# Kernel optimization log

Measured on AMD Instinct MI355X. Metric: run time of the kernel, lower is better.

Reference implementation:

```python
import jax, jax.numpy as jnp
import numpy as np

B, C, H, W = 4, 512, 64, 64
MID = C // 8  # 64


def setup_inputs() -> dict:
    key = jax.random.key(0)
    ks = jax.random.split(key, 8)
    s = 0.02
    return {
        "x": jax.random.normal(ks[0], (B, C, H, W), dtype=jnp.float32),
        "Wq": jax.random.normal(ks[1], (MID, C), dtype=jnp.float32) * s,
        "bq": jax.random.normal(ks[2], (MID,), dtype=jnp.float32) * s,
        "Wk": jax.random.normal(ks[3], (MID, C), dtype=jnp.float32) * s,
        "bk": jax.random.normal(ks[4], (MID,), dtype=jnp.float32) * s,
        "Wv": jax.random.normal(ks[5], (C, C), dtype=jnp.float32) * s,
        "bv": jax.random.normal(ks[6], (C,), dtype=jnp.float32) * s,
        "gamma": jax.random.uniform(ks[7], (1,), dtype=jnp.float32),
    }


def reference(x, Wq, bq, Wk, bk, Wv, bv, gamma):
    b, c, h, w = x.shape
    n = h * w
    xf = x.reshape(b, c, n)  # [B, C, N]
    # 1x1 convs are per-position linear maps
    q = jnp.einsum('mc,bcn->bnm', Wq, xf) + bq            # [B, N, mid]
    k = jnp.einsum('mc,bcn->bmn', Wk, xf) + bk[:, None]   # [B, mid, N]
    sim = jax.nn.softmax(jnp.einsum('bnm,bmj->bnj', q, k), axis=-1)  # [B, N, N]
    v = jnp.einsum('dc,bcn->bdn', Wv, xf) + bv[:, None]   # [B, C, N]
    # feat[:, d, i] = sum_j v[:, d, j] * sim[:, i, j]
    feat = jnp.einsum('bdj,bij->bdi', v, sim)             # [B, C, N]
    out = gamma[0] * feat + xf
    return out.reshape(b, c, h, w)
```

## Files before the change

### kernel.cpp

```cpp
#include <hip/hip_runtime.h>

#define BATCH 4
#define CCH   512
#define NN    4096
#define MIDD  64

typedef unsigned short u16;
typedef unsigned int   u32;
typedef short s8v  __attribute__((ext_vector_type(8)));
typedef float f16v __attribute__((ext_vector_type(16)));

__device__ __forceinline__ u16 f2bf(float f) {
  u32 u = __float_as_uint(f);
  u += 0x7fffu + ((u >> 16) & 1u);
  return (u16)(u >> 16);
}

__device__ __forceinline__ void g2lds16(const u16* g, u16* l) {
  __builtin_amdgcn_global_load_lds(
      (const __attribute__((address_space(1))) u32*)(const void*)g,
      (__attribute__((address_space(3))) u32*)(void*)l, 16, 0, 0);
}

#define S_WAITCNT(vm, lgkm) \
  __builtin_amdgcn_s_waitcnt(((vm) & 15) | (((vm) >> 4) << 14) | (0x7 << 4) | ((lgkm) << 8))

__global__ __launch_bounds__(256) void prep_w(
    const float* __restrict__ Wq, const float* __restrict__ Wk,
    const float* __restrict__ Wv, u16* __restrict__ Wb)
{
  int e = (blockIdx.x * 256 + threadIdx.x) * 8;
  const float* src;
  if (e < 64 * 512)       src = Wq + e;
  else if (e < 128 * 512) src = Wk + (e - 64 * 512);
  else                    src = Wv + (e - 128 * 512);
  float4 v0 = *(const float4*)src;
  float4 v1 = *(const float4*)(src + 4);
  uint4 p;
  p.x = (u32)f2bf(v0.x) | ((u32)f2bf(v0.y) << 16);
  p.y = (u32)f2bf(v0.z) | ((u32)f2bf(v0.w) << 16);
  p.z = (u32)f2bf(v1.x) | ((u32)f2bf(v1.y) << 16);
  p.w = (u32)f2bf(v1.z) | ((u32)f2bf(v1.w) << 16);
  *(uint4*)(Wb + e) = p;
}

__global__ __launch_bounds__(256) void transpose_cast(
    const float* __restrict__ x, u16* __restrict__ xbT)
{
  const int b  = blockIdx.z;
  const int c0 = blockIdx.y * 64;
  const int n0 = blockIdx.x * 64;
  const int t  = threadIdx.x;
  __shared__ float ts[64 * 65];

  #pragma unroll
  for (int k = 0; k < 4; k++) {
    int idx = t + 256 * k;
    int cc = idx >> 4, n4 = idx & 15;
    float4 v = *(const float4*)&x[((size_t)(b * CCH + c0 + cc)) * NN + n0 + n4 * 4];
    float* p = &ts[cc * 65 + n4 * 4];
    p[0] = v.x; p[1] = v.y; p[2] = v.z; p[3] = v.w;
  }
  __syncthreads();

  const int n = t >> 2, cb = (t & 3) * 16;
  u16 tmp[16];
  #pragma unroll
  for (int j = 0; j < 16; j++) tmp[j] = f2bf(ts[(cb + j) * 65 + n]);
  u16* dst = &xbT[((size_t)b * NN + n0 + n) * CCH + c0 + cb];
  *(uint4*)&dst[0] = *(uint4*)&tmp[0];
  *(uint4*)&dst[8] = *(uint4*)&tmp[8];
}

__global__ __launch_bounds__(256, 2) void proj_gemm(
    const u16* __restrict__ xbT, const u16* __restrict__ Wb,
    const float* __restrict__ bq, const float* __restrict__ bk,
    const float* __restrict__ bv,
    u16* __restrict__ qT, u16* __restrict__ kT, u16* __restrict__ vF)
{
  const int b  = blockIdx.z;
  const int mt = blockIdx.y;
  const int n0 = blockIdx.x * 256;
  const int t  = threadIdx.x;
  const int ln = t & 31, hi = (t & 63) >> 5, w = t >> 6;
  const int l  = t & 63;
  const int l2 = l & 3, lr = l >> 2;
  const int swc = (l2 ^ (lr & 3)) * 8;

  const int mrow0 = (mt < 8) ? (128 + mt * 64) : ((mt == 8) ? 0 : 64);
  const float* bias = (mt < 8) ? (bv + mt * 64) : ((mt == 8) ? bq : bk);

  __shared__ u16 ws[2][64 * 32];
  __shared__ u16 xs[2][256 * 32];

  const u16* xsrc = xbT + ((size_t)b * NN + n0 + w * 64 + lr) * CCH + swc;
  const u16* wsrc = Wb + (size_t)(mrow0 + w * 16 + lr) * 512 + swc;

  f16v acc[4];
  #pragma unroll
  for (int i = 0; i < 4; i++)
    #pragma unroll
    for (int r = 0; r < 16; r++) acc[i][r] = 0.f;

  #pragma unroll
  for (int i = 0; i < 4; i++)
    g2lds16(xsrc + (size_t)(16 * i) * CCH, &xs[0][(w * 64 + i * 16) * 32]);
  g2lds16(wsrc, &ws[0][w * 16 * 32]);

  for (int it = 0; it < 16; it++) {
    const int cur = it & 1, nxt = cur ^ 1;
    __builtin_amdgcn_s_barrier();
    const int c1 = ((it + 1) & 15) * 32;
    #pragma unroll
    for (int i = 0; i < 4; i++)
      g2lds16(xsrc + (size_t)(16 * i) * CCH + c1, &xs[nxt][(w * 64 + i * 16) * 32]);
    g2lds16(wsrc + c1, &ws[nxt][w * 16 * 32]);

    S_WAITCNT(5, 15);
    __builtin_amdgcn_s_barrier();

    #pragma unroll
    for (int ks = 0; ks < 2; ks++) {
      const int cb = ((2 * ks + hi) ^ (ln & 3)) << 3;
      s8v a0 = *(const s8v*)&ws[cur][(ln)           * 32 + cb];
      s8v a1 = *(const s8v*)&ws[cur][(32 + ln)      * 32 + cb];
      s8v b0 = *(const s8v*)&xs[cur][(w * 64 + ln)      * 32 + cb];
      s8v b1 = *(const s8v*)&xs[cur][(w * 64 + 32 + ln) * 32 + cb];
      acc[0] = __builtin_amdgcn_mfma_f32_32x32x16_bf16(a0, b0, acc[0], 0, 0, 0);
      acc[1] = __builtin_amdgcn_mfma_f32_32x32x16_bf16(a0, b1, acc[1], 0, 0, 0);
      acc[2] = __builtin_amdgcn_mfma_f32_32x32x16_bf16(a1, b0, acc[2], 0, 0, 0);
      acc[3] = __builtin_amdgcn_mfma_f32_32x32x16_bf16(a1, b1, acc[3], 0, 0, 0);
    }
  }

  S_WAITCNT(0, 0);
  __builtin_amdgcn_s_barrier();

  if (mt < 8) {
    u16* xt = &xs[0][0];
    #pragma unroll
    for (int mi = 0; mi < 2; mi++)
      #pragma unroll
      for (int ni = 0; ni < 2; ni++) {
        f16v& a = acc[mi * 2 + ni];
        #pragma unroll
        for (int r = 0; r < 16; r++) {
          int row = (r & 3) + 8 * (r >> 2) + 4 * hi;
          int m   = mi * 32 + row;
          int nr  = w * 64 + ni * 32 + ln;
          int c8  = nr >> 3;
          xt[m * 256 + ((c8 ^ (m & 31)) << 3) + (nr & 7)] = f2bf(a[r] + bias[m]);
        }
      }
    __syncthreads();
    const int jt0 = n0 >> 6;
    const size_t dgb = ((size_t)b * 64 + jt0 + w) * 16 + mt * 2;
    #pragma unroll
    for (int mh = 0; mh < 2; mh++)
      #pragma unroll
      for (int ks = 0; ks < 4; ks++) {
        int c8 = w * 8 + ks * 2 + hi;
        int m  = mh * 32 + ln;
        s8v vv = *(const s8v*)&xt[m * 256 + ((c8 ^ ln) << 3)];
        *(s8v*)&vF[(((dgb + mh) * 4 + ks) * 64 + l) * 8] = vv;
      }
  } else {
    u16* dst = (mt == 8) ? qT : kT;
    u16* xt  = &xs[0][0];
    #pragma unroll
    for (int mi = 0; mi < 2; mi++)
      #pragma unroll
      for (int ni = 0; ni < 2; ni++) {
        f16v& a = acc[mi * 2 + ni];
        #pragma unroll
        for (int r = 0; r < 16; r++) {
          int row = (r & 3) + 8 * (r >> 2) + 4 * hi;
          int m   = mi * 32 + row;
          int nr  = w * 64 + ni * 32 + ln;
          xt[(nr << 6) + (((m >> 3) ^ (ln & 7)) << 3) + (m & 7)] = f2bf(a[r] + bias[m]);
        }
      }
    __syncthreads();
    const int r7 = t & 7;
    u16* drow = &dst[((size_t)b * NN + n0 + t) * 64];
    #pragma unroll
    for (int k = 0; k < 8; k++)
      *(uint4*)&drow[k * 8] = *(uint4*)&xt[(t << 6) + ((k ^ r7) << 3)];
  }
}

__global__ __launch_bounds__(256, 2) void attn_kernel(
    const u16* __restrict__ qT,
    const u16* __restrict__ kT,
    const u16* __restrict__ vF,
    const float* __restrict__ x,
    const float* __restrict__ gamma,
    float* __restrict__ out)
{
  __shared__ u16 ksm[2][64 * 64];
  __shared__ u16 plm[2][64 * 64];

  const int bx    = blockIdx.x;
  const int slot  = bx & 7;
  const int b     = slot >> 1;
  const int dbase = (slot & 1) * 256;
  const int i0    = (bx >> 3) * 64;
  const int t     = threadIdx.x;
  const int l     = t & 63, ln = l & 31, hi = l >> 5;
  const int w     = t >> 6;
  const int qh    = w >> 1;
  const int jh    = w & 1;
  const int l3    = l & 7, lh3 = l >> 3;
  const int sw8   = (l3 ^ lh3) * 8;

  s8v qfrag[4];
  {
    const u16* qp = qT + ((size_t)b * NN + i0 + qh * 32 + ln) * 64 + hi * 8;
    #pragma unroll
    for (int k = 0; k < 4; k++) qfrag[k] = *(const s8v*)(qp + 16 * k);
  }

  const u16* kbase = kT + (size_t)b * NN * 64;
  const u16* ksrc  = kbase + (size_t)(16 * w + lh3) * 64 + sw8;
  const u16* vfb = vF + (size_t)b * (64 * 16 * 4 * 64 * 8);
  const int dg0  = (slot & 1) * 8 + w;

  f16v oacc[4];
  #pragma unroll
  for (int i = 0; i < 4; i++)
    #pragma unroll
    for (int r = 0; r < 16; r++) oacc[i][r] = 0.f;
  float lpart[16];
  #pragma unroll
  for (int r = 0; r < 16; r++) lpart[r] = 0.f;

  #pragma unroll
  for (int i = 0; i < 2; i++)
    g2lds16(ksrc + (size_t)(8 * i) * 64, &ksm[0][(w * 2 + i) * 512]);

  for (int it = 0; it < 64; it++) {
    const int cur = it & 1, nxt = cur ^ 1;

    s8v vf0[4], vf1[4];
    {
      const u16* vp0 = vfb + (size_t)(it * 16 + dg0) * (4 * 64 * 8) + l * 8;
      #pragma unroll
      for (int ks = 0; ks < 4; ks++) {
        vf0[ks] = *(const s8v*)(vp0 + ks * (64 * 8));
        vf1[ks] = *(const s8v*)(vp0 + 4 * (4 * 64 * 8) + ks * (64 * 8));
      }
    }

    const int j1 = ((it + 1) & 63) * 64;
    #pragma unroll
    for (int i = 0; i < 2; i++)
      g2lds16(ksrc + (size_t)(j1 + 8 * i) * 64, &ksm[nxt][(w * 2 + i) * 512]);

    S_WAITCNT(10, 15);
    __builtin_amdgcn_s_barrier();

    f16v sacc;
    #pragma unroll
    for (int r = 0; r < 16; r++) sacc[r] = 0.f;
    #pragma unroll
    for (int ks = 0; ks < 4; ks++) {
      s8v bf = *(const s8v*)&ksm[cur][(jh * 32 + ln) * 64 + (((2 * ks + hi) ^ l3) << 3)];
      sacc = __builtin_amdgcn_mfma_f32_32x32x16_bf16(qfrag[ks], bf, sacc, 0, 0, 0);
    }
    #pragma unroll
    for (int r = 0; r < 16; r++) {
      float p = __expf(sacc[r]);
      lpart[r] += p;
      int row = qh * 32 + (r & 3) + ((r >> 2) << 3) + (hi << 2);
      int r7  = (r & 3) + (hi << 2);
      int jbl = (jh << 2) + (ln >> 3);
      plm[cur][(row << 6) + ((jbl ^ r7) << 3) + (ln & 7)] = f2bf(p);
    }

    S_WAITCNT(2, 0);
    __builtin_amdgcn_s_barrier();

    #pragma unroll
    for (int ks = 0; ks < 4; ks++) {
      const int cb = ((2 * ks + hi) ^ l3) << 3;
      s8v p0 = *(const s8v*)&plm[cur][(ln << 6) + cb];
      s8v p1 = *(const s8v*)&plm[cur][((32 + ln) << 6) + cb];
      oacc[0] = __builtin_amdgcn_mfma_f32_32x32x16_bf16(vf0[ks], p0, oacc[0], 0, 0, 0);
      oacc[1] = __builtin_amdgcn_mfma_f32_32x32x16_bf16(vf0[ks], p1, oacc[1], 0, 0, 0);
      oacc[2] = __builtin_amdgcn_mfma_f32_32x32x16_bf16(vf1[ks], p0, oacc[2], 0, 0, 0);
      oacc[3] = __builtin_amdgcn_mfma_f32_32x32x16_bf16(vf1[ks], p1, oacc[3], 0, 0, 0);
    }
  }

  S_WAITCNT(0, 0);
  __builtin_amdgcn_s_barrier();

  float* lred = (float*)&ksm[0][0];
  #pragma unroll
  for (int r = 0; r < 16; r++) {
    float v = lpart[r];
    v += __shfl_xor(v, 1);  v += __shfl_xor(v, 2);  v += __shfl_xor(v, 4);
    v += __shfl_xor(v, 8);  v += __shfl_xor(v, 16);
    lpart[r] = v;
  }
  if (ln == 0) {
    #pragma unroll
    for (int r = 0; r < 16; r++) {
      int row = qh * 32 + (r & 3) + ((r >> 2) << 3) + (hi << 2);
      lred[jh * 64 + row] = lpart[r];
    }
  }
  __syncthreads();

  const float g0 = gamma[0];
  #pragma unroll
  for (int qt = 0; qt < 2; qt++) {
    const float linv = 1.0f / (lred[qt * 32 + ln] + lred[64 + qt * 32 + ln]);
    const int n = i0 + qt * 32 + ln;
    #pragma unroll
    for (int ds = 0; ds < 2; ds++) {
      f16v& a = oacc[ds * 2 + qt];
      const int dg = dbase + (w + 4 * ds) * 32;
      #pragma unroll
      for (int r = 0; r < 16; r++) {
        int dl = (r & 3) + 8 * (r >> 2) + 4 * hi;
        size_t idx = ((size_t)b * CCH + dg + dl) * NN + n;
        out[idx] = g0 * a[r] * linv + x[idx];
      }
    }
  }
}

extern "C" void kernel_launch(void* const* d_in, const int* in_sizes, int n_in,
                              void* d_out, int out_size, void* d_ws, size_t ws_size,
                              hipStream_t stream) {
  const float* x     = (const float*)d_in[0];
  const float* Wq    = (const float*)d_in[1];
  const float* bq    = (const float*)d_in[2];
  const float* Wk    = (const float*)d_in[3];
  const float* bk    = (const float*)d_in[4];
  const float* Wv    = (const float*)d_in[5];
  const float* bv    = (const float*)d_in[6];
  const float* gamma = (const float*)d_in[7];
  float* out = (float*)d_out;

  u16* qT  = (u16*)d_ws;
  u16* kT  = qT  + (size_t)BATCH * NN * MIDD;
  u16* vF  = kT  + (size_t)BATCH * NN * MIDD;
  u16* xbT = vF  + (size_t)BATCH * CCH * NN;
  u16* Wb  = xbT + (size_t)BATCH * NN * CCH;

  prep_w<<<dim3(160), 256, 0, stream>>>(Wq, Wk, Wv, Wb);
  transpose_cast<<<dim3(NN / 64, CCH / 64, BATCH), 256, 0, stream>>>(x, xbT);
  proj_gemm<<<dim3(NN / 256, 10, BATCH), 256, 0, stream>>>(
      xbT, Wb, bq, bk, bv, qT, kT, vF);
  attn_kernel<<<dim3(512), 256, 0, stream>>>(qT, kT, vF, x, gamma, out);
}
```

Measured before the change: 223.9 us.

## Keep softmax probabilities in registers via transposed QK and lane shuffles

Each wave now computes S^T (K as the A operand, Q as B) for its own 32 queries across all 64 keys. It converts exp(S) to bf16 and rearranges it with cross-half lane shuffles so it can feed the PV MFMA directly as the B operand. This removes the LDS round-trip for P, one barrier per iteration, and the end-of-kernel row-sum reduction through LDS. K is also triple-buffered in LDS with a two-tile prefetch distance, and each wave loads 16 V fragments per iteration instead of 8. The costs are more register pressure, two QK MFMAs per wave where one was enough before, and twice the global V traffic per wave.

```diff
diff --git a/kernel.cpp b/kernel.cpp
--- a/kernel.cpp
+++ b/kernel.cpp
@@ -9,6 +9,7 @@
 typedef unsigned int   u32;
 typedef short s8v  __attribute__((ext_vector_type(8)));
 typedef float f16v __attribute__((ext_vector_type(16)));
+typedef unsigned int u4v __attribute__((ext_vector_type(4)));
 
 __device__ __forceinline__ u16 f2bf(float f) {
   u32 u = __float_as_uint(f);
@@ -197,8 +198,7 @@
     const float* __restrict__ gamma,
     float* __restrict__ out)
 {
-  __shared__ u16 ksm[2][64 * 64];
-  __shared__ u16 plm[2][64 * 64];
+  __shared__ u16 ksm[3][64 * 64];
 
   const int bx    = blockIdx.x;
   const int slot  = bx & 7;
@@ -208,8 +208,8 @@
   const int t     = threadIdx.x;
   const int l     = t & 63, ln = l & 31, hi = l >> 5;
   const int w     = t >> 6;
-  const int qh    = w >> 1;
-  const int jh    = w & 1;
+  const int qh    = w & 1;
+  const int dh    = w >> 1;
   const int l3    = l & 7, lh3 = l >> 3;
   const int sw8   = (l3 ^ lh3) * 8;
 
@@ -220,113 +220,110 @@
     for (int k = 0; k < 4; k++) qfrag[k] = *(const s8v*)(qp + 16 * k);
   }
 
-  const u16* kbase = kT + (size_t)b * NN * 64;
-  const u16* ksrc  = kbase + (size_t)(16 * w + lh3) * 64 + sw8;
+  const u16* ksrc = kT + (size_t)b * NN * 64 + (size_t)(16 * w + lh3) * 64 + sw8;
   const u16* vfb = vF + (size_t)b * (64 * 16 * 4 * 64 * 8);
-  const int dg0  = (slot & 1) * 8 + w;
+  const int dgbase = (slot & 1) * 8 + dh * 4;
 
   f16v oacc[4];
   #pragma unroll
   for (int i = 0; i < 4; i++)
     #pragma unroll
     for (int r = 0; r < 16; r++) oacc[i][r] = 0.f;
-  float lpart[16];
-  #pragma unroll
-  for (int r = 0; r < 16; r++) lpart[r] = 0.f;
+  float lsum = 0.f;
 
   #pragma unroll
   for (int i = 0; i < 2; i++)
     g2lds16(ksrc + (size_t)(8 * i) * 64, &ksm[0][(w * 2 + i) * 512]);
-
+  #pragma unroll
+  for (int i = 0; i < 2; i++)
+    g2lds16(ksrc + (size_t)(64 + 8 * i) * 64, &ksm[1][(w * 2 + i) * 512]);
+
+  int cur = 0, nx1 = 1, nx2 = 2;
   for (int it = 0; it < 64; it++) {
-    const int cur = it & 1, nxt = cur ^ 1;
-
-    s8v vf0[4], vf1[4];
+    s8v vf[4][4];
     {
-      const u16* vp0 = vfb + (size_t)(it * 16 + dg0) * (4 * 64 * 8) + l * 8;
+      const u16* vp = vfb + (size_t)(it * 16 + dgbase) * 2048 + l * 8;
+      #pragma unroll
+      for (int dgi = 0; dgi < 4; dgi++)
+        #pragma unroll
+        for (int ks = 0; ks < 4; ks++)
+          vf[dgi][ks] = *(const s8v*)(vp + dgi * 2048 + ks * 512);
+    }
+
+    S_WAITCNT(16, 15);
+    __builtin_amdgcn_s_barrier();
+
+    {
+      const int j2 = ((it + 2) & 63) * 64;
+      u16* kdst = &ksm[0][0] + nx2 * 4096 + (w * 2) * 512;
+      #pragma unroll
+      for (int i = 0; i < 2; i++)
+        g2lds16(ksrc + (size_t)(j2 + 8 * i) * 64, kdst + i * 512);
+    }
+
+    const u16* kcur = &ksm[0][0] + cur * 4096;
+    f16v ssw[2];
+    #pragma unroll
+    for (int jh2 = 0; jh2 < 2; jh2++) {
+      #pragma unroll
+      for (int r = 0; r < 16; r++) ssw[jh2][r] = 0.f;
       #pragma unroll
       for (int ks = 0; ks < 4; ks++) {
-        vf0[ks] = *(const s8v*)(vp0 + ks * (64 * 8));
-        vf1[ks] = *(const s8v*)(vp0 + 4 * (4 * 64 * 8) + ks * (64 * 8));
-      }
-    }
-
-    const int j1 = ((it + 1) & 63) * 64;
-    #pragma unroll
-    for (int i = 0; i < 2; i++)
-      g2lds16(ksrc + (size_t)(j1 + 8 * i) * 64, &ksm[nxt][(w * 2 + i) * 512]);
-
-    S_WAITCNT(10, 15);
-    __builtin_amdgcn_s_barrier();
-
-    f16v sacc;
-    #pragma unroll
-    for (int r = 0; r < 16; r++) sacc[r] = 0.f;
+        s8v kf = *(const s8v*)&kcur[(jh2 * 32 + ln) * 64 + (((2 * ks + hi) ^ l3) << 3)];
+        ssw[jh2] = __builtin_amdgcn_mfma_f32_32x32x16_bf16(kf, qfrag[ks], ssw[jh2], 0, 0, 0);
+      }
+    }
+
+    u4v pfq[4];
+    #pragma unroll
+    for (int a2 = 0; a2 < 2; a2++) {
+      float pe[16];
+      #pragma unroll
+      for (int r = 0; r < 16; r++) {
+        pe[r] = __expf(ssw[a2][r]);
+        lsum += pe[r];
+      }
+      #pragma unroll
+      for (int b2 = 0; b2 < 2; b2++)
+        #pragma unroll
+        for (int wd = 0; wd < 2; wd++) {
+          u32 X = (u32)f2bf(pe[8 * b2 + 2 * wd])
+                | ((u32)f2bf(pe[8 * b2 + 2 * wd + 1]) << 16);
+          u32 Y = (u32)f2bf(pe[8 * b2 + 4 + 2 * wd])
+                | ((u32)f2bf(pe[8 * b2 + 4 + 2 * wd + 1]) << 16);
+          u32 Xs = (u32)__shfl_xor((int)X, 32);
+          u32 Ys = (u32)__shfl_xor((int)Y, 32);
+          pfq[a2 * 2 + b2][wd]     = hi ? Ys : X;
+          pfq[a2 * 2 + b2][wd + 2] = hi ? Y  : Xs;
+        }
+    }
+
     #pragma unroll
     for (int ks = 0; ks < 4; ks++) {
-      s8v bf = *(const s8v*)&ksm[cur][(jh * 32 + ln) * 64 + (((2 * ks + hi) ^ l3) << 3)];
-      sacc = __builtin_amdgcn_mfma_f32_32x32x16_bf16(qfrag[ks], bf, sacc, 0, 0, 0);
-    }
+      s8v pb = (s8v)pfq[ks];
+      oacc[0] = __builtin_amdgcn_mfma_f32_32x32x16_bf16(vf[0][ks], pb, oacc[0], 0, 0, 0);
+      oacc[1] = __builtin_amdgcn_mfma_f32_32x32x16_bf16(vf[1][ks], pb, oacc[1], 0, 0, 0);
+      oacc[2] = __builtin_amdgcn_mfma_f32_32x32x16_bf16(vf[2][ks], pb, oacc[2], 0, 0, 0);
+      oacc[3] = __builtin_amdgcn_mfma_f32_32x32x16_bf16(vf[3][ks], pb, oacc[3], 0, 0, 0);
+    }
+
+    int tmp = cur; cur = nx1; nx1 = nx2; nx2 = tmp;
+  }
+
+  S_WAITCNT(0, 0);
+
+  const float lt   = lsum + __shfl_xor(lsum, 32);
+  const float linv = 1.0f / lt;
+  const float g0   = gamma[0];
+  const int   q    = i0 + qh * 32 + ln;
+  #pragma unroll
+  for (int dgi = 0; dgi < 4; dgi++) {
+    f16v& a = oacc[dgi];
     #pragma unroll
     for (int r = 0; r < 16; r++) {
-      float p = __expf(sacc[r]);
-      lpart[r] += p;
-      int row = qh * 32 + (r & 3) + ((r >> 2) << 3) + (hi << 2);
-      int r7  = (r & 3) + (hi << 2);
-      int jbl = (jh << 2) + (ln >> 3);
-      plm[cur][(row << 6) + ((jbl ^ r7) << 3) + (ln & 7)] = f2bf(p);
-    }
-
-    S_WAITCNT(2, 0);
-    __builtin_amdgcn_s_barrier();
-
-    #pragma unroll
-    for (int ks = 0; ks < 4; ks++) {
-      const int cb = ((2 * ks + hi) ^ l3) << 3;
-      s8v p0 = *(const s8v*)&plm[cur][(ln << 6) + cb];
-      s8v p1 = *(const s8v*)&plm[cur][((32 + ln) << 6) + cb];
-      oacc[0] = __builtin_amdgcn_mfma_f32_32x32x16_bf16(vf0[ks], p0, oacc[0], 0, 0, 0);
-      oacc[1] = __builtin_amdgcn_mfma_f32_32x32x16_bf16(vf0[ks], p1, oacc[1], 0, 0, 0);
-      oacc[2] = __builtin_amdgcn_mfma_f32_32x32x16_bf16(vf1[ks], p0, oacc[2], 0, 0, 0);
-      oacc[3] = __builtin_amdgcn_mfma_f32_32x32x16_bf16(vf1[ks], p1, oacc[3], 0, 0, 0);
-    }
-  }
-
-  S_WAITCNT(0, 0);
-  __builtin_amdgcn_s_barrier();
-
-  float* lred = (float*)&ksm[0][0];
-  #pragma unroll
-  for (int r = 0; r < 16; r++) {
-    float v = lpart[r];
-    v += __shfl_xor(v, 1);  v += __shfl_xor(v, 2);  v += __shfl_xor(v, 4);
-    v += __shfl_xor(v, 8);  v += __shfl_xor(v, 16);
-    lpart[r] = v;
-  }
-  if (ln == 0) {
-    #pragma unroll
-    for (int r = 0; r < 16; r++) {
-      int row = qh * 32 + (r & 3) + ((r >> 2) << 3) + (hi << 2);
-      lred[jh * 64 + row] = lpart[r];
-    }
-  }
-  __syncthreads();
-
-  const float g0 = gamma[0];
-  #pragma unroll
-  for (int qt = 0; qt < 2; qt++) {
-    const float linv = 1.0f / (lred[qt * 32 + ln] + lred[64 + qt * 32 + ln]);
-    const int n = i0 + qt * 32 + ln;
-    #pragma unroll
-    for (int ds = 0; ds < 2; ds++) {
-      f16v& a = oacc[ds * 2 + qt];
-      const int dg = dbase + (w + 4 * ds) * 32;
-      #pragma unroll
-      for (int r = 0; r < 16; r++) {
-        int dl = (r & 3) + 8 * (r >> 2) + 4 * hi;
-        size_t idx = ((size_t)b * CCH + dg + dl) * NN + n;
-        out[idx] = g0 * a[r] * linv + x[idx];
-      }
+      int dl = dh * 128 + dgi * 32 + (r & 3) + 8 * (r >> 2) + 4 * hi;
+      size_t idx = ((size_t)b * CCH + dbase + dl) * NN + q;
+      out[idx] = g0 * a[r] * linv + x[idx];
     }
   }
 }
```

Result: slower. 252.5 us (+12.8%).
